# Kernel tuning notes

Measured on AMD Instinct MI355X. Metric: run time of the kernel, lower is better.

## Reference

```python
import jax, jax.numpy as jnp
import numpy as np

WS = (7, 7)   # window size
SS = (3, 3)   # shift size
NH = 8        # num heads
DIM = 256
B_, H_, W_ = 16, 112, 112


def _rel_index(wh, ww):
    ch, cw = np.meshgrid(np.arange(wh), np.arange(ww), indexing='ij')
    cf = np.stack([ch, cw]).reshape(2, -1)
    rc = (cf[:, :, None] - cf[:, None, :]).transpose(1, 2, 0)
    rc[:, :, 0] += wh - 1
    rc[:, :, 1] += ww - 1
    rc[:, :, 0] *= 2 * ww - 1
    return rc.sum(-1).reshape(-1)


def _shift_mask(pH, pW, wh, ww, sh, sw):
    m = np.zeros((pH, pW))
    cnt = 0
    for h0, h1 in ((0, pH - wh), (pH - wh, pH - sh), (pH - sh, pH)):
        for w0, w1 in ((0, pW - ww), (pW - ww, pW - sw), (pW - sw, pW)):
            m[h0:h1, w0:w1] = cnt
            cnt += 1
    m = m.reshape(pH // wh, wh, pW // ww, ww).transpose(0, 2, 1, 3).reshape(-1, wh * ww)
    d = m[:, None, :] - m[:, :, None]  # (nW, N, N), [w,i,j] = m[w,j]-m[w,i]
    return np.where(d != 0, -100.0, 0.0).astype(np.float32)


def _partition(x, wh, ww):
    B, H, W, C = x.shape
    x = x.reshape(B, H // wh, wh, W // ww, ww, C).transpose(0, 1, 3, 2, 4, 5)
    return x.reshape(B * (H // wh) * (W // ww), wh * ww, C)


def _unpartition(x, B, H, W, wh, ww):
    C = x.shape[-1]
    x = x.reshape(B, H // wh, W // ww, wh, ww, C).transpose(0, 1, 3, 2, 4, 5)
    return x.reshape(B, H, W, C)


def setup_inputs() -> dict:
    key = jax.random.key(0)
    ks = jax.random.split(key, 12)
    D = DIM
    inp = {
        'Q': jax.random.normal(ks[0], (B_, H_, W_, D), jnp.float32),
        'K': jax.random.normal(ks[1], (B_, H_, W_, D), jnp.float32),
        'V': jax.random.normal(ks[2], (B_, H_, W_, D), jnp.float32),
        'Qw': jax.random.normal(ks[3], (D, D), jnp.float32) * 0.02,
        'Qb': jax.random.normal(ks[4], (D,), jnp.float32) * 0.02,
        'Kw': jax.random.normal(ks[5], (D, D), jnp.float32) * 0.02,
        'Kb': jax.random.normal(ks[6], (D,), jnp.float32) * 0.02,
        'Vw': jax.random.normal(ks[7], (D, D), jnp.float32) * 0.02,
        'Vb': jax.random.normal(ks[8], (D,), jnp.float32) * 0.02,
        'Pw': jax.random.normal(ks[9], (D, D), jnp.float32) * 0.02,
        'Pb': jax.random.normal(ks[10], (D,), jnp.float32) * 0.02,
        'rpb_table': jax.random.normal(ks[11], ((2 * WS[0] - 1) * (2 * WS[1] - 1), NH), jnp.float32) * 0.02,
        'rp_index': jnp.asarray(_rel_index(WS[0], WS[1]), jnp.int32),
    }
    return inp


def reference(Q, K, V, Qw, Qb, Kw, Kb, Vw, Vb, Pw, Pb, rpb_table, rp_index):
    wh, ww = WS
    nh = NH
    B, H, W, C = Q.shape
    N = wh * ww
    hd = C // nh
    pad_b = (wh - H % wh) % wh
    pad_r = (ww - W % ww) % ww
    if pad_b or pad_r:
        pad = ((0, 0), (0, pad_b), (0, pad_r), (0, 0))
        Q, K, V = jnp.pad(Q, pad), jnp.pad(K, pad), jnp.pad(V, pad)
    pH, pW = H + pad_b, W + pad_r
    sh = 0 if wh >= pH else SS[0]
    sw = 0 if ww >= pW else SS[1]
    shifted = (sh + sw) > 0
    if shifted:
        Q = jnp.roll(Q, (-sh, -sw), (1, 2))
        K = jnp.roll(K, (-sh, -sw), (1, 2))
        V = jnp.roll(V, (-sh, -sw), (1, 2))
    xq = _partition(Q, wh, ww)  # (B*nW, N, C)
    xk = _partition(K, wh, ww)
    xv = _partition(V, wh, ww)
    q = (xq @ Qw.T + Qb).reshape(-1, N, nh, hd).transpose(0, 2, 1, 3) * (hd ** -0.5)
    k = (xk @ Kw.T + Kb).reshape(-1, N, nh, hd).transpose(0, 2, 1, 3)
    v = (xv @ Vw.T + Vb).reshape(-1, N, nh, hd).transpose(0, 2, 1, 3)
    bias = rpb_table[rp_index].reshape(N, N, nh).transpose(2, 0, 1)  # (nh, N, N)
    attn = jnp.einsum('bhnd,bhmd->bhnm', q, k) + bias[None]
    if shifted:
        mask = jnp.asarray(_shift_mask(pH, pW, wh, ww, sh, sw))  # (nW, N, N)
        nW = (pH // wh) * (pW // ww)
        attn = attn.reshape(B, nW, nh, N, N) + mask[None, :, None]
        attn = attn.reshape(-1, nh, N, N)
    attn = jax.nn.softmax(attn, axis=-1)
    x = jnp.einsum('bhnm,bhmd->bhnd', attn, v).transpose(0, 2, 1, 3).reshape(-1, N, C)
    x = x @ Pw.T + Pb
    x = _unpartition(x, B, pH, pW, wh, ww)
    if shifted:
        x = jnp.roll(x, (sh, sw), (1, 2))
    return x[:, :H, :W, :]
```

## Files before the change

kernel.cpp:

```cpp
#include <hip/hip_runtime.h>


typedef short  bf16x4_t __attribute__((ext_vector_type(4)));
typedef short  bf16x8_t __attribute__((ext_vector_type(8)));
typedef float  f32x4_t  __attribute__((ext_vector_type(4)));
typedef int    i32x4_t  __attribute__((ext_vector_type(4)));

#define HH    112
#define WWDIM 112
#define NTOK  49
#define NWIN  4096
#define SHIFT 3
#define LOG2E 1.4426950408889634f
#define MASKS (-144.26950408889634f)

__device__ __forceinline__ unsigned short f2bf(float f) {
  unsigned u = __builtin_bit_cast(unsigned, f);
  u += 0x7FFFu + ((u >> 16) & 1u);
  return (unsigned short)(u >> 16);
}

__device__ __forceinline__ unsigned cvtpk(float a, float b) {
  unsigned r;
  asm("v_cvt_pk_bf16_f32 %0, %1, %2" : "=v"(r) : "v"(a), "v"(b));
  return r;
}

__device__ __forceinline__ float exp2fast(float x) {
  float r;
  asm("v_exp_f32 %0, %1" : "=v"(r) : "v"(x));
  return r;
}

__device__ __forceinline__ bf16x8_t ld8(const unsigned short* p) {
  return __builtin_bit_cast(bf16x8_t, *reinterpret_cast<const i32x4_t*>(p));
}

__device__ __forceinline__ bf16x4_t pack4(float a, float b, float c, float d) {
  union { unsigned u[2]; bf16x4_t v; } t;
  t.u[0] = cvtpk(a, b); t.u[1] = cvtpk(c, d);
  return t.v;
}

__device__ __forceinline__ int swzi(int row, int col, int rowElems) {
  int by = col << 1;
  int sb = (((by >> 4) ^ (row & 7)) << 4) | (by & 15);
  return row * rowElems + (sb >> 1);
}

__global__ void prep_kernel(const float* __restrict__ Qw, const float* __restrict__ Kw,
                            const float* __restrict__ Vw, const float* __restrict__ Pw,
                            const float* __restrict__ rpb, const int* __restrict__ rpi,
                            unsigned short* __restrict__ wbf, float* __restrict__ biasP) {
  int idx = blockIdx.x * 256 + threadIdx.x;
  if (idx < 4 * 65536) {
    int which = idx >> 16, e = idx & 65535;
    const float* s = (which == 0) ? Qw : (which == 1) ? Kw : (which == 2) ? Vw : Pw;
    wbf[idx] = f2bf(s[e]);
  }
  if (idx < 8 * 49 * 64) {
    int h = idx / 3136, r = idx - h * 3136;
    int i = r >> 6, j = r & 63;
    biasP[idx] = (i < NTOK && j < NTOK) ? rpb[rpi[i * NTOK + j] * 8 + h] * LOG2E : 0.f;
  }
}

#define GLOAD(SRC)                                                            \
  do {                                                                        \
    _Pragma("unroll") for (int it = 0; it < 16; ++it) {                       \
      g[it] = (((it << 2) + wid) < NTOK)                                      \
                  ? *reinterpret_cast<const float4*>((SRC) + goff[it])        \
                  : make_float4(0.f, 0.f, 0.f, 0.f);                          \
    }                                                                         \
  } while (0)

#define XWRITE(B)                                                             \
  do {                                                                        \
    _Pragma("unroll") for (int it = 0; it < 16; ++it) {                       \
      unsigned v0 = cvtpk(g[it].x, g[it].y);                                  \
      unsigned v1 = cvtpk(g[it].z, g[it].w);                                  \
      *reinterpret_cast<uint2*>(                                              \
          &Xs[B][swzi((it << 2) + wid, lane << 2, 256)]) = make_uint2(v0, v1);\
    }                                                                         \
  } while (0)

#define WLOAD(WP, KS, S)                                                      \
  do {                                                                        \
    _Pragma("unroll") for (int m = 0; m < 4; ++m)                             \
      bwr[S][m] = ld8(&(WP)[(((wid << 6) + (m << 4) + lo) << 8) +             \
                            ((KS) << 5) + kof]);                              \
  } while (0)

__global__ __launch_bounds__(256, 2) void fused_kernel(
    const float* __restrict__ Qin, const float* __restrict__ Kin, const float* __restrict__ Vin,
    const float* __restrict__ Qbv, const float* __restrict__ Kbv, const float* __restrict__ Vbv,
    const float* __restrict__ Pbv,
    const unsigned short* __restrict__ wbf, const float* __restrict__ biasP,
    float* __restrict__ out) {
  __shared__ unsigned short Xs[2][64 * 256];

  const int blk = blockIdx.x, tid = threadIdx.x;
  const int lane = tid & 63, wid = tid >> 6;
  const int b = blk >> 8, wi = (blk >> 4) & 15, wj = blk & 15;
  const int lo = lane & 15, hi = lane >> 4;
  const int g4 = hi << 2, kof = hi << 3;

  unsigned goff[16];
#pragma unroll
  for (int it = 0; it < 16; ++it) {
    int row = (it << 2) + wid;
    unsigned off = 0;
    if (row < NTOK) {
      int i = row / 7, j = row - i * 7;
      int h_ = wi * 7 + i + SHIFT; if (h_ >= HH) h_ -= HH;
      int w_ = wj * 7 + j + SHIFT; if (w_ >= WWDIM) w_ -= WWDIM;
      off = ((unsigned)((b * HH + h_) * WWDIM + w_) << 8) + (lane << 2);
    }
    goff[it] = off;
  }

  float4 g[16];
  bf16x8_t bwr[2][4];
  bf16x4_t qf[4][4], kf[4][4], vf[4][4];

  GLOAD(Qin);
  XWRITE(0);
  __syncthreads();

#pragma unroll
  for (int ph = 0; ph < 2; ++ph) {
    GLOAD(ph == 0 ? Kin : Vin);
    const unsigned short* Xb = Xs[ph];
    const unsigned short* W_ = wbf + (ph << 16);
    f32x4_t acc[4][4];
#pragma unroll
    for (int a = 0; a < 4; ++a)
#pragma unroll
      for (int c = 0; c < 4; ++c) acc[a][c] = (f32x4_t){0.f, 0.f, 0.f, 0.f};
    WLOAD(W_, 0, 0);
#pragma unroll
    for (int ks = 0; ks < 8; ++ks) {
      if (ks < 7) WLOAD(W_, ks + 1, (ks + 1) & 1);
      const int kk = (ks << 5) + kof;
      bf16x8_t xb[4];
#pragma unroll
      for (int nj = 0; nj < 4; ++nj) xb[nj] = ld8(&Xb[swzi((nj << 4) + lo, kk, 256)]);
#pragma unroll
      for (int m = 0; m < 4; ++m)
#pragma unroll
        for (int nj = 0; nj < 4; ++nj)
          acc[m][nj] = __builtin_amdgcn_mfma_f32_16x16x32_bf16(bwr[ks & 1][m], xb[nj], acc[m][nj], 0, 0, 0);
    }
    const float* bias = (ph == 0) ? Qbv : Kbv;
    const float scale = (ph == 0) ? 0.17677669529663687f * LOG2E : 1.0f;
#pragma unroll
    for (int m = 0; m < 4; ++m) {
      const float4 bb = *reinterpret_cast<const float4*>(bias + (wid << 6) + (m << 4) + g4);
#pragma unroll
      for (int nj = 0; nj < 4; ++nj) {
        const bf16x4_t v = pack4((acc[m][nj][0] + bb.x) * scale, (acc[m][nj][1] + bb.y) * scale,
                                 (acc[m][nj][2] + bb.z) * scale, (acc[m][nj][3] + bb.w) * scale);
        if (ph == 0) qf[m][nj] = v; else kf[m][nj] = v;
      }
    }
    XWRITE(ph ^ 1);
    __syncthreads();
  }

  {
    const unsigned short* Xb = Xs[0];
    const unsigned short* W_ = wbf + (2 << 16);
    f32x4_t acc[4][4];
#pragma unroll
    for (int a = 0; a < 4; ++a)
#pragma unroll
      for (int c = 0; c < 4; ++c) acc[a][c] = (f32x4_t){0.f, 0.f, 0.f, 0.f};
    WLOAD(W_, 0, 0);
#pragma unroll
    for (int ks = 0; ks < 8; ++ks) {
      if (ks < 7) WLOAD(W_, ks + 1, (ks + 1) & 1);
      const int kk = (ks << 5) + kof;
      bf16x8_t xa[4];
#pragma unroll
      for (int mi = 0; mi < 4; ++mi) xa[mi] = ld8(&Xb[swzi((mi << 4) + lo, kk, 256)]);
#pragma unroll
      for (int mi = 0; mi < 4; ++mi)
#pragma unroll
        for (int t = 0; t < 4; ++t)
          acc[mi][t] = __builtin_amdgcn_mfma_f32_16x16x32_bf16(xa[mi], bwr[ks & 1][t], acc[mi][t], 0, 0, 0);
    }
    float bbv[4];
#pragma unroll
    for (int t = 0; t < 4; ++t) bbv[t] = Vbv[(wid << 6) + (t << 4) + lo];
#pragma unroll
    for (int mi = 0; mi < 4; ++mi)
#pragma unroll
      for (int t = 0; t < 4; ++t)
        vf[mi][t] = pack4(acc[mi][t][0] + bbv[t], acc[mi][t][1] + bbv[t],
                          acc[mi][t][2] + bbv[t], acc[mi][t][3] + bbv[t]);
  }

  const bool wi15 = (wi == 15), wj15 = (wj == 15);
  unsigned kbi = 0, kbj = 0, kval = 0;
#pragma unroll
  for (int njk = 0; njk < 4; ++njk)
#pragma unroll
    for (int rg = 0; rg < 4; ++rg) {
      int kt = (njk << 4) + g4 + rg;
      if (kt < NTOK) {
        int ti = kt / 7, tj = kt - (kt / 7) * 7;
        unsigned bit = 1u << (njk * 4 + rg);
        kval |= bit;
        if (ti >= 4) kbi |= bit;
        if (tj >= 4) kbj |= bit;
      }
    }

#pragma unroll
  for (int hh = 0; hh < 2; ++hh) {
    const int h = (wid << 1) + hh;
    const int co = h << 5;

    bf16x4_t pf[4][4];
#pragma unroll
    for (int njq = 0; njq < 4; ++njq) {
      const int qt = (njq << 4) + lo;
      const bool qv = qt < NTOK;
      const int sqt = qv ? qt : 0;
      const float* bq = biasP + h * 3136 + (sqt << 6);
      f32x4_t bfr[4];
#pragma unroll
      for (int njk = 0; njk < 4; ++njk)
        bfr[njk] = *reinterpret_cast<const f32x4_t*>(bq + (njk << 4) + g4);

      f32x4_t stc[4];
      __builtin_amdgcn_s_setprio(1);
#pragma unroll
      for (int njk = 0; njk < 4; ++njk) {
        stc[njk] = __builtin_amdgcn_mfma_f32_16x16x16bf16_1k(
            kf[(hh << 1)][njk], qf[(hh << 1)][njq], (f32x4_t){0.f, 0.f, 0.f, 0.f}, 0, 0, 0);
        stc[njk] = __builtin_amdgcn_mfma_f32_16x16x16bf16_1k(
            kf[(hh << 1) + 1][njk], qf[(hh << 1) + 1][njq], stc[njk], 0, 0, 0);
      }
      __builtin_amdgcn_s_setprio(0);

      const int qti = sqt / 7, qtj = sqt - (sqt / 7) * 7;
      const bool qbi = qti >= 4, qbj = qtj >= 4;
      float m = -3e38f;
#pragma unroll
      for (int njk = 0; njk < 4; ++njk)
#pragma unroll
        for (int rg = 0; rg < 4; ++rg) {
          const int bit = njk * 4 + rg;
          const bool valid = qv && ((kval >> bit) & 1u);
          float v = stc[njk][rg] + bfr[njk][rg];
          if (wi15 && (qbi != (bool)((kbi >> bit) & 1u))) v += MASKS;
          if (wj15 && (qbj != (bool)((kbj >> bit) & 1u))) v += MASKS;
          v = valid ? v : -1e30f;
          stc[njk][rg] = v;
          m = fmaxf(m, v);
        }
      m = fmaxf(m, __shfl_xor(m, 16));
      m = fmaxf(m, __shfl_xor(m, 32));
      float sum = 0.f;
#pragma unroll
      for (int njk = 0; njk < 4; ++njk)
#pragma unroll
        for (int rg = 0; rg < 4; ++rg) {
          const float e = exp2fast(stc[njk][rg] - m);
          stc[njk][rg] = e;
          sum += e;
        }
      sum += __shfl_xor(sum, 16);
      sum += __shfl_xor(sum, 32);
      const float inv = __builtin_amdgcn_rcpf(sum);
#pragma unroll
      for (int njk = 0; njk < 4; ++njk)
        pf[njk][njq] = pack4(stc[njk][0] * inv, stc[njk][1] * inv,
                             stc[njk][2] * inv, stc[njk][3] * inv);
    }

    f32x4_t o[2][4];
#pragma unroll
    for (int a = 0; a < 2; ++a)
#pragma unroll
      for (int c = 0; c < 4; ++c) o[a][c] = (f32x4_t){0.f, 0.f, 0.f, 0.f};
    __builtin_amdgcn_s_setprio(1);
#pragma unroll
    for (int mi = 0; mi < 4; ++mi)
#pragma unroll
      for (int t2 = 0; t2 < 2; ++t2)
#pragma unroll
        for (int njq = 0; njq < 4; ++njq)
          o[t2][njq] = __builtin_amdgcn_mfma_f32_16x16x16bf16_1k(
              vf[mi][(hh << 1) + t2], pf[mi][njq], o[t2][njq], 0, 0, 0);
    __builtin_amdgcn_s_setprio(0);

#pragma unroll
    for (int t2 = 0; t2 < 2; ++t2)
#pragma unroll
      for (int njq = 0; njq < 4; ++njq) {
        const int qt = (njq << 4) + lo;
        const int ch0 = co + (t2 << 4) + g4;
        *reinterpret_cast<uint2*>(&Xs[1][swzi(qt, ch0, 256)]) =
            make_uint2(cvtpk(o[t2][njq][0], o[t2][njq][1]),
                       cvtpk(o[t2][njq][2], o[t2][njq][3]));
      }
  }
  __syncthreads();

  {
    const unsigned short* Xb = Xs[1];
    const unsigned short* W_ = wbf + (3 << 16);
    f32x4_t y[4][4];
#pragma unroll
    for (int a = 0; a < 4; ++a)
#pragma unroll
      for (int c = 0; c < 4; ++c) y[a][c] = (f32x4_t){0.f, 0.f, 0.f, 0.f};
    WLOAD(W_, 0, 0);
#pragma unroll
    for (int ks = 0; ks < 8; ++ks) {
      if (ks < 7) WLOAD(W_, ks + 1, (ks + 1) & 1);
      const int kk = (ks << 5) + kof;
      bf16x8_t xb[4];
#pragma unroll
      for (int nj = 0; nj < 4; ++nj) xb[nj] = ld8(&Xb[swzi((nj << 4) + lo, kk, 256)]);
#pragma unroll
      for (int m = 0; m < 4; ++m)
#pragma unroll
        for (int nj = 0; nj < 4; ++nj)
          y[m][nj] = __builtin_amdgcn_mfma_f32_16x16x32_bf16(bwr[ks & 1][m], xb[nj], y[m][nj], 0, 0, 0);
    }
#pragma unroll
    for (int nj = 0; nj < 4; ++nj) {
      const int tok = (nj << 4) + lo;
      if (tok < NTOK) {
        const int i = tok / 7, j = tok - (tok / 7) * 7;
        int h_ = wi * 7 + i + SHIFT; if (h_ >= HH) h_ -= HH;
        int w_ = wj * 7 + j + SHIFT; if (w_ >= WWDIM) w_ -= WWDIM;
        float* ob = out + ((size_t)((b * HH + h_) * WWDIM + w_) << 8);
#pragma unroll
        for (int m = 0; m < 4; ++m) {
          const int ch0 = (wid << 6) + (m << 4) + g4;
          const float4 pb = *reinterpret_cast<const float4*>(Pbv + ch0);
          *reinterpret_cast<float4*>(ob + ch0) =
              make_float4(y[m][nj][0] + pb.x, y[m][nj][1] + pb.y,
                          y[m][nj][2] + pb.z, y[m][nj][3] + pb.w);
        }
      }
    }
  }
}

extern "C" void kernel_launch(void* const* d_in, const int* in_sizes, int n_in,
                              void* d_out, int out_size, void* d_ws, size_t ws_size,
                              hipStream_t stream) {
  const float* Q   = (const float*)d_in[0];
  const float* K   = (const float*)d_in[1];
  const float* V   = (const float*)d_in[2];
  const float* Qw  = (const float*)d_in[3];
  const float* Qb  = (const float*)d_in[4];
  const float* Kw  = (const float*)d_in[5];
  const float* Kb  = (const float*)d_in[6];
  const float* Vw  = (const float*)d_in[7];
  const float* Vb  = (const float*)d_in[8];
  const float* Pw  = (const float*)d_in[9];
  const float* Pb  = (const float*)d_in[10];
  const float* rpb = (const float*)d_in[11];
  const int*   rpi = (const int*)d_in[12];

  unsigned short* wbf = (unsigned short*)d_ws;
  float* biasP = (float*)(wbf + 4 * 65536);

  const size_t need = (size_t)4 * 65536 * 2 + (size_t)8 * 49 * 64 * 4;
  if (ws_size < need) return;

  prep_kernel<<<1024, 256, 0, stream>>>(Qw, Kw, Vw, Pw, rpb, rpi, wbf, biasP);
  fused_kernel<<<NWIN, 256, 0, stream>>>(Q, K, V, Qb, Kb, Vb, Pb, wbf, biasP,
                                         (float*)d_out);
}
```

Baseline: 445.5 us.

## Stage fp32 Q/K/V tiles directly into LDS via global_load_lds with single buffer

Replaces the register-staged global loads plus bf16 conversion and LDS write with direct global-to-LDS DMA (global_load_lds) of raw fp32 rows into a single XOR-swizzled fp32 buffer. Conversion to bf16 now happens at fragment read time. The double buffer is dropped, so the next input's load is issued only after the current projection finishes, with extra barriers. This frees the 16 float4 staging registers and VALU conversion work, but it loses the overlap of the next load with the current GEMM and doubles the LDS bytes read per fragment. Rows beyond token 49 are no longer zero-filled and read stale data, which only reaches the padded columns.

Result: faster. 410.2 us (-7.9%).

```diff
diff --git a/kernel.cpp b/kernel.cpp
--- a/kernel.cpp
+++ b/kernel.cpp
@@ -39,6 +39,23 @@
 __device__ __forceinline__ bf16x4_t pack4(float a, float b, float c, float d) {
   union { unsigned u[2]; bf16x4_t v; } t;
   t.u[0] = cvtpk(a, b); t.u[1] = cvtpk(c, d);
+  return t.v;
+}
+
+__device__ __forceinline__ void gload16(const float* g, float* l) {
+  __builtin_amdgcn_global_load_lds(
+      (const __attribute__((address_space(1))) void*)g,
+      (__attribute__((address_space(3))) void*)l, 16, 0, 0);
+}
+
+__device__ __forceinline__ bf16x8_t ldx(const float* Xf, int tok, int kk) {
+  const int base = tok << 8;
+  const int cs = (((kk >> 2) ^ (tok & 7)) << 2);
+  const f32x4_t a = *reinterpret_cast<const f32x4_t*>(Xf + base + cs);
+  const f32x4_t c = *reinterpret_cast<const f32x4_t*>(Xf + base + (cs ^ 4));
+  union { unsigned u[4]; bf16x8_t v; } t;
+  t.u[0] = cvtpk(a[0], a[1]); t.u[1] = cvtpk(a[2], a[3]);
+  t.u[2] = cvtpk(c[0], c[1]); t.u[3] = cvtpk(c[2], c[3]);
   return t.v;
 }
 
@@ -65,22 +82,12 @@
   }
 }
 
-#define GLOAD(SRC)                                                            \
+#define GSTAGE(SRC)                                                           \
   do {                                                                        \
     _Pragma("unroll") for (int it = 0; it < 16; ++it) {                       \
-      g[it] = (((it << 2) + wid) < NTOK)                                      \
-                  ? *reinterpret_cast<const float4*>((SRC) + goff[it])        \
-                  : make_float4(0.f, 0.f, 0.f, 0.f);                          \
-    }                                                                         \
-  } while (0)
-
-#define XWRITE(B)                                                             \
-  do {                                                                        \
-    _Pragma("unroll") for (int it = 0; it < 16; ++it) {                       \
-      unsigned v0 = cvtpk(g[it].x, g[it].y);                                  \
-      unsigned v1 = cvtpk(g[it].z, g[it].w);                                  \
-      *reinterpret_cast<uint2*>(                                              \
-          &Xs[B][swzi((it << 2) + wid, lane << 2, 256)]) = make_uint2(v0, v1);\
+      const int row = wid + (it << 2);                                        \
+      gload16((SRC) + goff[it] + ((it & 1) ? (f0 ^ 16) : f0),                 \
+              Xf + (row << 8));                                               \
     }                                                                         \
   } while (0)
 
@@ -97,40 +104,38 @@
     const float* __restrict__ Pbv,
     const unsigned short* __restrict__ wbf, const float* __restrict__ biasP,
     float* __restrict__ out) {
-  __shared__ unsigned short Xs[2][64 * 256];
+  __shared__ float Xf[64 * 256];
+  unsigned short* Ab = (unsigned short*)Xf;
 
   const int blk = blockIdx.x, tid = threadIdx.x;
   const int lane = tid & 63, wid = tid >> 6;
   const int b = blk >> 8, wi = (blk >> 4) & 15, wj = blk & 15;
   const int lo = lane & 15, hi = lane >> 4;
   const int g4 = hi << 2, kof = hi << 3;
+  const int f0 = (lane ^ wid) << 2;
 
   unsigned goff[16];
 #pragma unroll
   for (int it = 0; it < 16; ++it) {
-    int row = (it << 2) + wid;
+    int row = wid + (it << 2);
     unsigned off = 0;
     if (row < NTOK) {
       int i = row / 7, j = row - i * 7;
       int h_ = wi * 7 + i + SHIFT; if (h_ >= HH) h_ -= HH;
       int w_ = wj * 7 + j + SHIFT; if (w_ >= WWDIM) w_ -= WWDIM;
-      off = ((unsigned)((b * HH + h_) * WWDIM + w_) << 8) + (lane << 2);
+      off = ((unsigned)((b * HH + h_) * WWDIM + w_) << 8);
     }
     goff[it] = off;
   }
 
-  float4 g[16];
   bf16x8_t bwr[2][4];
   bf16x4_t qf[4][4], kf[4][4], vf[4][4];
 
-  GLOAD(Qin);
-  XWRITE(0);
+  GSTAGE(Qin);
   __syncthreads();
 
 #pragma unroll
   for (int ph = 0; ph < 2; ++ph) {
-    GLOAD(ph == 0 ? Kin : Vin);
-    const unsigned short* Xb = Xs[ph];
     const unsigned short* W_ = wbf + (ph << 16);
     f32x4_t acc[4][4];
 #pragma unroll
@@ -144,13 +149,16 @@
       const int kk = (ks << 5) + kof;
       bf16x8_t xb[4];
 #pragma unroll
-      for (int nj = 0; nj < 4; ++nj) xb[nj] = ld8(&Xb[swzi((nj << 4) + lo, kk, 256)]);
+      for (int nj = 0; nj < 4; ++nj) xb[nj] = ldx(Xf, (nj << 4) + lo, kk);
 #pragma unroll
       for (int m = 0; m < 4; ++m)
 #pragma unroll
         for (int nj = 0; nj < 4; ++nj)
           acc[m][nj] = __builtin_amdgcn_mfma_f32_16x16x32_bf16(bwr[ks & 1][m], xb[nj], acc[m][nj], 0, 0, 0);
     }
+    __syncthreads();
+    GSTAGE(ph == 0 ? Kin : Vin);
+
     const float* bias = (ph == 0) ? Qbv : Kbv;
     const float scale = (ph == 0) ? 0.17677669529663687f * LOG2E : 1.0f;
 #pragma unroll
@@ -163,12 +171,10 @@
         if (ph == 0) qf[m][nj] = v; else kf[m][nj] = v;
       }
     }
-    XWRITE(ph ^ 1);
     __syncthreads();
   }
 
   {
-    const unsigned short* Xb = Xs[0];
     const unsigned short* W_ = wbf + (2 << 16);
     f32x4_t acc[4][4];
 #pragma unroll
@@ -182,13 +188,14 @@
       const int kk = (ks << 5) + kof;
       bf16x8_t xa[4];
 #pragma unroll
-      for (int mi = 0; mi < 4; ++mi) xa[mi] = ld8(&Xb[swzi((mi << 4) + lo, kk, 256)]);
+      for (int mi = 0; mi < 4; ++mi) xa[mi] = ldx(Xf, (mi << 4) + lo, kk);
 #pragma unroll
       for (int mi = 0; mi < 4; ++mi)
 #pragma unroll
         for (int t = 0; t < 4; ++t)
           acc[mi][t] = __builtin_amdgcn_mfma_f32_16x16x32_bf16(xa[mi], bwr[ks & 1][t], acc[mi][t], 0, 0, 0);
     }
+    __syncthreads();
     float bbv[4];
 #pragma unroll
     for (int t = 0; t < 4; ++t) bbv[t] = Vbv[(wid << 6) + (t << 4) + lo];
@@ -302,7 +309,7 @@
       for (int njq = 0; njq < 4; ++njq) {
         const int qt = (njq << 4) + lo;
         const int ch0 = co + (t2 << 4) + g4;
-        *reinterpret_cast<uint2*>(&Xs[1][swzi(qt, ch0, 256)]) =
+        *reinterpret_cast<uint2*>(&Ab[swzi(qt, ch0, 256)]) =
             make_uint2(cvtpk(o[t2][njq][0], o[t2][njq][1]),
                        cvtpk(o[t2][njq][2], o[t2][njq][3]));
       }
@@ -310,7 +317,6 @@
   __syncthreads();
 
   {
-    const unsigned short* Xb = Xs[1];
     const unsigned short* W_ = wbf + (3 << 16);
     f32x4_t y[4][4];
 #pragma unroll
@@ -324,7 +330,7 @@
       const int kk = (ks << 5) + kof;
       bf16x8_t xb[4];
 #pragma unroll
-      for (int nj = 0; nj < 4; ++nj) xb[nj] = ld8(&Xb[swzi((nj << 4) + lo, kk, 256)]);
+      for (int nj = 0; nj < 4; ++nj) xb[nj] = ld8(&Ab[swzi((nj << 4) + lo, kk, 256)]);
 #pragma unroll
       for (int m = 0; m < 4; ++m)
 #pragma unroll
```
